# Optimization experiments

Measured on AMD Instinct MI355X. Metric: run time of the kernel, lower is better.

## Reference

```python
import jax, jax.numpy as jnp
import numpy as np

B, C, N = 4, 192, 4096
K = 16                      # avg degree
E = B * N * K               # 262144 edges
C_OUT = 384


def setup_inputs() -> dict:
    key = jax.random.key(0)
    k1, k2, k3, k4 = jax.random.split(key, 4)
    x = jax.random.normal(k1, (B, C, N, 1), dtype=jnp.float32)
    edge_index = jax.random.randint(k2, (2, E), 0, B * N, dtype=jnp.int64)
    # BasicConv([2C, C_OUT]): 1x1 Conv2d + bias + ReLU (norm=None)
    W = jax.random.normal(k3, (C_OUT, 2 * C), dtype=jnp.float32) * (1.0 / np.sqrt(2 * C))
    b = jax.random.normal(k4, (C_OUT,), dtype=jnp.float32) * 0.01
    return {"x": x, "edge_index": edge_index, "W": W, "b": b}


def reference(x, edge_index, W, b):
    Bs, Cs, Ns, _ = x.shape
    BN = Bs * Ns
    # (B,C,N,1) -> flattened node table (B*N, C); node id = b*N + n
    x_flat = jnp.transpose(x[..., 0], (0, 2, 1)).reshape(BN, Cs)
    x_i = x_flat[edge_index[0]]          # (E, C) gather at dst
    x_j = x_flat[edge_index[1]]          # (E, C) gather at src
    diff = x_j - x_i
    # scatter-max over dst nodes; torch_scatter fills empty segments with 0
    agg = jax.ops.segment_max(diff, edge_index[0], num_segments=BN)
    agg = jnp.where(jnp.isfinite(agg), agg, 0.0)
    x_j_out = jnp.transpose(agg.reshape(Bs, Ns, Cs), (0, 2, 1))[..., None]  # (B,C,N,1)
    # interleave channels: cat along new axis 2 then reshape -> (B, 2C, N, 1)
    cat = jnp.stack([x, x_j_out], axis=2).reshape(Bs, 2 * Cs, Ns, 1)
    # 1x1 conv == GEMM over channels, + bias + ReLU
    out = jnp.einsum('oc,bcnw->bonw', W, cat) + b[None, :, None, None]
    return jax.nn.relu(out)
```

## Files before the change

### kernel.cpp

```cpp
#include <hip/hip_runtime.h>
#include <hip/hip_bf16.h>
#include <math.h>

#define Bz    4
#define Cch   192
#define Nn    4096
#define BN    16384
#define Ecnt  262144
#define COUT  384
#define CAP   64

typedef __attribute__((ext_vector_type(8))) short short8;
typedef __attribute__((ext_vector_type(4))) float floatx4;

__device__ __forceinline__ void gload_lds16(const void* g, void* l) {
    __builtin_amdgcn_global_load_lds(
        (const __attribute__((address_space(1))) unsigned int*)g,
        (__attribute__((address_space(3))) unsigned int*)l, 16, 0, 0);
}

__device__ __forceinline__ float b2f(unsigned short u) {
    union { unsigned int i; float f; } z; z.i = ((unsigned int)u) << 16; return z.f;
}
__device__ __forceinline__ unsigned short f2b(float f) {
    __hip_bfloat16 h = __float2bfloat16(f);
    return *(unsigned short*)&h;
}

__global__ __launch_bounds__(256) void prep_kernel(
    const float* __restrict__ x, const unsigned int* __restrict__ ew,
    const float* __restrict__ W, __hip_bfloat16* __restrict__ xb,
    __hip_bfloat16* __restrict__ Wx, __hip_bfloat16* __restrict__ Wa,
    int* __restrict__ deg, int* __restrict__ flag) {
    int bid = blockIdx.x;
    if (bid < 3072) {
        __shared__ float tile[32][33];
        int b = bid / 768;
        int r = bid - b * 768;
        int c0 = (r >> 7) * 32;
        int n0 = (r & 127) * 32;
        int tx = threadIdx.x & 31, ty = threadIdx.x >> 5;
        for (int i = ty; i < 32; i += 8)
            tile[i][tx] = x[((size_t)(b * Cch + c0 + i)) * Nn + n0 + tx];
        __syncthreads();
        for (int i = ty; i < 32; i += 8)
            xb[((size_t)(b * Nn + n0 + i)) * Cch + c0 + tx] =
                __float2bfloat16(tile[tx][i]);
    } else if (bid < 3360) {
        int i = (bid - 3072) * 256 + threadIdx.x;
        int o = i / Cch, c = i - o * Cch;
        Wx[i] = __float2bfloat16(W[o * 2 * Cch + 2 * c]);
        Wa[i] = __float2bfloat16(W[o * 2 * Cch + 2 * c + 1]);
    } else if (bid < 3424) {
        deg[(bid - 3360) * 256 + threadIdx.x] = 0;
    } else {
        __shared__ int s;
        if (threadIdx.x == 0) s = 1;
        __syncthreads();
        if (ew[2 * threadIdx.x + 1] != 0u) atomicAnd(&s, 0);
        __syncthreads();
        if (threadIdx.x == 0) *flag = s;
    }
}

__global__ __launch_bounds__(256) void fill_kernel(
    const int* __restrict__ ew, const int* __restrict__ flag,
    int* __restrict__ deg, int* __restrict__ slots) {
    int t = blockIdx.x * 256 + threadIdx.x;
    int d0, d1, s0, s1;
    if (*flag) {
        int4 dv = *(const int4*)&ew[4 * t];
        int4 sv = *(const int4*)&ew[2 * Ecnt + 4 * t];
        d0 = dv.x; d1 = dv.z; s0 = sv.x; s1 = sv.z;
    } else {
        int2 dv = *(const int2*)&ew[2 * t];
        int2 sv = *(const int2*)&ew[Ecnt + 2 * t];
        d0 = dv.x; d1 = dv.y; s0 = sv.x; s1 = sv.y;
    }
    int p0 = atomicAdd(&deg[d0], 1); if (p0 < CAP) slots[(d0 << 6) + p0] = s0;
    int p1 = atomicAdd(&deg[d1], 1); if (p1 < CAP) slots[(d1 << 6) + p1] = s1;
}

__global__ __launch_bounds__(256) void agg_kernel(
    const int* __restrict__ deg, const int* __restrict__ slots,
    const __hip_bfloat16* __restrict__ xb, __hip_bfloat16* __restrict__ aggb) {
    int lane = threadIdx.x & 63, wave = threadIdx.x >> 6;
    int node = (blockIdx.x << 2) + wave;
    int d = deg[node]; if (d > CAP) d = CAP;
    int nbrval = 0;
    if (lane < d) nbrval = slots[(node << 6) + lane];
    const unsigned short* xbu = (const unsigned short*)xb;
    int act = lane < 48;
    int cb = lane * 4;
    float m0 = -INFINITY, m1 = -INFINITY, m2 = -INFINITY, m3 = -INFINITY;
    int k = 0;
    for (; k + 4 <= d; k += 4) {
        int s0 = __shfl(nbrval, k);
        int s1 = __shfl(nbrval, k + 1);
        int s2 = __shfl(nbrval, k + 2);
        int s3 = __shfl(nbrval, k + 3);
        if (act) {
            ushort4 v0 = *(const ushort4*)&xbu[s0 * Cch + cb];
            ushort4 v1 = *(const ushort4*)&xbu[s1 * Cch + cb];
            ushort4 v2 = *(const ushort4*)&xbu[s2 * Cch + cb];
            ushort4 v3 = *(const ushort4*)&xbu[s3 * Cch + cb];
            m0 = fmaxf(fmaxf(m0, b2f(v0.x)), fmaxf(fmaxf(b2f(v1.x), b2f(v2.x)), b2f(v3.x)));
            m1 = fmaxf(fmaxf(m1, b2f(v0.y)), fmaxf(fmaxf(b2f(v1.y), b2f(v2.y)), b2f(v3.y)));
            m2 = fmaxf(fmaxf(m2, b2f(v0.z)), fmaxf(fmaxf(b2f(v1.z), b2f(v2.z)), b2f(v3.z)));
            m3 = fmaxf(fmaxf(m3, b2f(v0.w)), fmaxf(fmaxf(b2f(v1.w), b2f(v2.w)), b2f(v3.w)));
        }
    }
    for (; k < d; k++) {
        int s = __shfl(nbrval, k);
        if (act) {
            ushort4 v = *(const ushort4*)&xbu[s * Cch + cb];
            m0 = fmaxf(m0, b2f(v.x)); m1 = fmaxf(m1, b2f(v.y));
            m2 = fmaxf(m2, b2f(v.z)); m3 = fmaxf(m3, b2f(v.w));
        }
    }
    if (act) {
        ushort4 xv = *(const ushort4*)&xbu[node * Cch + cb];
        ushort4 o4;
        o4.x = (d > 0) ? f2b(m0 - b2f(xv.x)) : 0;
        o4.y = (d > 0) ? f2b(m1 - b2f(xv.y)) : 0;
        o4.z = (d > 0) ? f2b(m2 - b2f(xv.z)) : 0;
        o4.w = (d > 0) ? f2b(m3 - b2f(xv.w)) : 0;
        *(ushort4*)&((unsigned short*)aggb)[node * Cch + cb] = o4;
    }
}

__global__ __launch_bounds__(256) void gemm_kernel(
    const __hip_bfloat16* __restrict__ Xb, const __hip_bfloat16* __restrict__ Ab,
    const __hip_bfloat16* __restrict__ Wx, const __hip_bfloat16* __restrict__ Wa,
    const float* __restrict__ bias, float* __restrict__ out) {
    __shared__ short As[64 * 32];
    __shared__ short Bs[64 * 32];
    int t = threadIdx.x;
    int node0 = blockIdx.x * 64;
    int o0    = blockIdx.y * 64;
    int lane = t & 63, wave = t >> 6;
    int quad = lane >> 4, lrow = lane & 15;
    int wm = wave & 1, wn = wave >> 1;

    floatx4 acc[2][2] = {};
    int srow = t >> 2;
    int koff = (t & 3) * 8;

    const __hip_bfloat16* Asrc[2] = {Xb, Ab};
    const __hip_bfloat16* Bsrc[2] = {Wx, Wa};

    for (int seg = 0; seg < 2; seg++) {
        const __hip_bfloat16* a_g = Asrc[seg] + (size_t)(node0 + srow) * Cch + koff;
        const __hip_bfloat16* b_g = Bsrc[seg] + (size_t)(o0 + srow) * Cch + koff;
        for (int kt = 0; kt < Cch; kt += 32) {
            __syncthreads();
            gload_lds16(a_g + kt, &As[t * 8]);
            gload_lds16(b_g + kt, &Bs[t * 8]);
            __syncthreads();
            short8 af0 = *(const short8*)&As[(wm * 32 + lrow) * 32 + quad * 8];
            short8 af1 = *(const short8*)&As[(wm * 32 + 16 + lrow) * 32 + quad * 8];
            short8 bf0 = *(const short8*)&Bs[(wn * 32 + lrow) * 32 + quad * 8];
            short8 bf1 = *(const short8*)&Bs[(wn * 32 + 16 + lrow) * 32 + quad * 8];
            acc[0][0] = __builtin_amdgcn_mfma_f32_16x16x32_bf16(bf0, af0, acc[0][0], 0, 0, 0);
            acc[1][0] = __builtin_amdgcn_mfma_f32_16x16x32_bf16(bf0, af1, acc[1][0], 0, 0, 0);
            acc[0][1] = __builtin_amdgcn_mfma_f32_16x16x32_bf16(bf1, af0, acc[0][1], 0, 0, 0);
            acc[1][1] = __builtin_amdgcn_mfma_f32_16x16x32_bf16(bf1, af1, acc[1][1], 0, 0, 0);
        }
    }

#pragma unroll
    for (int im = 0; im < 2; im++) {
        int node = node0 + wm * 32 + im * 16 + lrow;
        int b = node >> 12, n = node & 4095;
#pragma unroll
        for (int in = 0; in < 2; in++) {
            int ob = o0 + wn * 32 + in * 16 + quad * 4;
#pragma unroll
            for (int r = 0; r < 4; r++) {
                int o = ob + r;
                float v = acc[im][in][r] + bias[o];
                out[((size_t)(b * COUT + o)) * Nn + n] = fmaxf(v, 0.0f);
            }
        }
    }
}

extern "C" void kernel_launch(void* const* d_in, const int* in_sizes, int n_in,
                              void* d_out, int out_size, void* d_ws, size_t ws_size,
                              hipStream_t stream) {
    const float* x    = (const float*)d_in[0];
    const int*   ew   = (const int*)d_in[1];
    const float* W    = (const float*)d_in[2];
    const float* bias = (const float*)d_in[3];
    float* out        = (float*)d_out;

    char* ws = (char*)d_ws;
    __hip_bfloat16* xb   = (__hip_bfloat16*)ws;
    __hip_bfloat16* aggb = (__hip_bfloat16*)(ws + 6291456);
    __hip_bfloat16* Wx   = (__hip_bfloat16*)(ws + 12582912);
    __hip_bfloat16* Wa   = (__hip_bfloat16*)(ws + 12730368);
    int* deg   = (int*)(ws + 12877824);
    int* slots = (int*)(ws + 12943360);
    int* flag  = (int*)(ws + 17137664);

    prep_kernel<<<3425, 256, 0, stream>>>(x, (const unsigned int*)ew, W, xb, Wx, Wa, deg, flag);
    fill_kernel<<<Ecnt / 512, 256, 0, stream>>>(ew, flag, deg, slots);
    agg_kernel<<<BN / 4, 256, 0, stream>>>(deg, slots, xb, aggb);
    gemm_kernel<<<dim3(BN / 64, COUT / 64), 256, 0, stream>>>(xb, aggb, Wx, Wa, bias, out);
}
```

Before: 115.8 us.

## Fuse aggregation into GEMM via LDS and merge prep with edge fill

Each block now computes the max-aggregated neighbour features for its 64 nodes directly into a padded LDS tile and loops over all six output tiles, so the aggb buffer is never written to or read back from global memory. Edge slot filling moves into the prep kernel, with the format check done per block, and deg is zeroed by a memset, reducing four launches to two plus a memset. The GEMM grid shrinks from 1536 to 256 blocks with about 55KB of LDS each, which lowers parallelism and occupancy during the gather phase. The fill blocks now run in the same kernel as the x transpose that writes xb, but only the aggregation reads xb, so there is no race.

```diff
diff --git a/kernel.cpp b/kernel.cpp
--- a/kernel.cpp
+++ b/kernel.cpp
@@ -9,6 +9,7 @@
 #define Ecnt  262144
 #define COUT  384
 #define CAP   64
+#define PADW  392
 
 typedef __attribute__((ext_vector_type(8))) short short8;
 typedef __attribute__((ext_vector_type(4))) float floatx4;
@@ -27,11 +28,11 @@
     return *(unsigned short*)&h;
 }
 
-__global__ __launch_bounds__(256) void prep_kernel(
-    const float* __restrict__ x, const unsigned int* __restrict__ ew,
+__global__ __launch_bounds__(256) void prep_fill_kernel(
+    const float* __restrict__ x, const int* __restrict__ ew,
     const float* __restrict__ W, __hip_bfloat16* __restrict__ xb,
     __hip_bfloat16* __restrict__ Wx, __hip_bfloat16* __restrict__ Wa,
-    int* __restrict__ deg, int* __restrict__ flag) {
+    int* __restrict__ deg, int* __restrict__ slots) {
     int bid = blockIdx.x;
     if (bid < 3072) {
         __shared__ float tile[32][33];
@@ -51,111 +52,106 @@
         int o = i / Cch, c = i - o * Cch;
         Wx[i] = __float2bfloat16(W[o * 2 * Cch + 2 * c]);
         Wa[i] = __float2bfloat16(W[o * 2 * Cch + 2 * c + 1]);
-    } else if (bid < 3424) {
-        deg[(bid - 3360) * 256 + threadIdx.x] = 0;
     } else {
         __shared__ int s;
         if (threadIdx.x == 0) s = 1;
         __syncthreads();
-        if (ew[2 * threadIdx.x + 1] != 0u) atomicAnd(&s, 0);
+        if (((const unsigned int*)ew)[2 * threadIdx.x + 1] != 0u) atomicAnd(&s, 0);
         __syncthreads();
-        if (threadIdx.x == 0) *flag = s;
+        int is64 = s;
+        int t = (bid - 3360) * 256 + threadIdx.x;
+        int d0, d1, s0, s1;
+        if (is64) {
+            int4 dv = *(const int4*)&ew[4 * t];
+            int4 sv = *(const int4*)&ew[2 * Ecnt + 4 * t];
+            d0 = dv.x; d1 = dv.z; s0 = sv.x; s1 = sv.z;
+        } else {
+            int2 dv = *(const int2*)&ew[2 * t];
+            int2 sv = *(const int2*)&ew[Ecnt + 2 * t];
+            d0 = dv.x; d1 = dv.y; s0 = sv.x; s1 = sv.y;
+        }
+        int p0 = atomicAdd(&deg[d0], 1); if (p0 < CAP) slots[(d0 << 6) + p0] = s0;
+        int p1 = atomicAdd(&deg[d1], 1); if (p1 < CAP) slots[(d1 << 6) + p1] = s1;
     }
 }
 
-__global__ __launch_bounds__(256) void fill_kernel(
-    const int* __restrict__ ew, const int* __restrict__ flag,
-    int* __restrict__ deg, int* __restrict__ slots) {
-    int t = blockIdx.x * 256 + threadIdx.x;
-    int d0, d1, s0, s1;
-    if (*flag) {
-        int4 dv = *(const int4*)&ew[4 * t];
-        int4 sv = *(const int4*)&ew[2 * Ecnt + 4 * t];
-        d0 = dv.x; d1 = dv.z; s0 = sv.x; s1 = sv.z;
-    } else {
-        int2 dv = *(const int2*)&ew[2 * t];
-        int2 sv = *(const int2*)&ew[Ecnt + 2 * t];
-        d0 = dv.x; d1 = dv.y; s0 = sv.x; s1 = sv.y;
-    }
-    int p0 = atomicAdd(&deg[d0], 1); if (p0 < CAP) slots[(d0 << 6) + p0] = s0;
-    int p1 = atomicAdd(&deg[d1], 1); if (p1 < CAP) slots[(d1 << 6) + p1] = s1;
-}
-
-__global__ __launch_bounds__(256) void agg_kernel(
+__global__ __launch_bounds__(256) void agg_gemm_kernel(
     const int* __restrict__ deg, const int* __restrict__ slots,
-    const __hip_bfloat16* __restrict__ xb, __hip_bfloat16* __restrict__ aggb) {
-    int lane = threadIdx.x & 63, wave = threadIdx.x >> 6;
-    int node = (blockIdx.x << 2) + wave;
-    int d = deg[node]; if (d > CAP) d = CAP;
-    int nbrval = 0;
-    if (lane < d) nbrval = slots[(node << 6) + lane];
-    const unsigned short* xbu = (const unsigned short*)xb;
-    int act = lane < 48;
-    int cb = lane * 4;
-    float m0 = -INFINITY, m1 = -INFINITY, m2 = -INFINITY, m3 = -INFINITY;
-    int k = 0;
-    for (; k + 4 <= d; k += 4) {
-        int s0 = __shfl(nbrval, k);
-        int s1 = __shfl(nbrval, k + 1);
-        int s2 = __shfl(nbrval, k + 2);
-        int s3 = __shfl(nbrval, k + 3);
-        if (act) {
-            ushort4 v0 = *(const ushort4*)&xbu[s0 * Cch + cb];
-            ushort4 v1 = *(const ushort4*)&xbu[s1 * Cch + cb];
-            ushort4 v2 = *(const ushort4*)&xbu[s2 * Cch + cb];
-            ushort4 v3 = *(const ushort4*)&xbu[s3 * Cch + cb];
-            m0 = fmaxf(fmaxf(m0, b2f(v0.x)), fmaxf(fmaxf(b2f(v1.x), b2f(v2.x)), b2f(v3.x)));
-            m1 = fmaxf(fmaxf(m1, b2f(v0.y)), fmaxf(fmaxf(b2f(v1.y), b2f(v2.y)), b2f(v3.y)));
-            m2 = fmaxf(fmaxf(m2, b2f(v0.z)), fmaxf(fmaxf(b2f(v1.z), b2f(v2.z)), b2f(v3.z)));
-            m3 = fmaxf(fmaxf(m3, b2f(v0.w)), fmaxf(fmaxf(b2f(v1.w), b2f(v2.w)), b2f(v3.w)));
-        }
-    }
-    for (; k < d; k++) {
-        int s = __shfl(nbrval, k);
-        if (act) {
-            ushort4 v = *(const ushort4*)&xbu[s * Cch + cb];
-            m0 = fmaxf(m0, b2f(v.x)); m1 = fmaxf(m1, b2f(v.y));
-            m2 = fmaxf(m2, b2f(v.z)); m3 = fmaxf(m3, b2f(v.w));
-        }
-    }
-    if (act) {
-        ushort4 xv = *(const ushort4*)&xbu[node * Cch + cb];
-        ushort4 o4;
-        o4.x = (d > 0) ? f2b(m0 - b2f(xv.x)) : 0;
-        o4.y = (d > 0) ? f2b(m1 - b2f(xv.y)) : 0;
-        o4.z = (d > 0) ? f2b(m2 - b2f(xv.z)) : 0;
-        o4.w = (d > 0) ? f2b(m3 - b2f(xv.w)) : 0;
-        *(ushort4*)&((unsigned short*)aggb)[node * Cch + cb] = o4;
-    }
-}
-
-__global__ __launch_bounds__(256) void gemm_kernel(
-    const __hip_bfloat16* __restrict__ Xb, const __hip_bfloat16* __restrict__ Ab,
+    const __hip_bfloat16* __restrict__ xb,
     const __hip_bfloat16* __restrict__ Wx, const __hip_bfloat16* __restrict__ Wa,
     const float* __restrict__ bias, float* __restrict__ out) {
+    __shared__ unsigned short aggT[64 * PADW];
     __shared__ short As[64 * 32];
     __shared__ short Bs[64 * 32];
     int t = threadIdx.x;
+    int lane = t & 63, wave = t >> 6;
     int node0 = blockIdx.x * 64;
-    int o0    = blockIdx.y * 64;
-    int lane = t & 63, wave = t >> 6;
+
+    {
+        const unsigned short* xbu = (const unsigned short*)xb;
+        int act = lane < 48;
+        int cb = lane * 4;
+        for (int it = 0; it < 16; it++) {
+            int nl = wave * 16 + it;
+            int node = node0 + nl;
+            int d = deg[node]; if (d > CAP) d = CAP;
+            int nbrval = 0;
+            if (lane < d) nbrval = slots[(node << 6) + lane];
+            float m0 = -INFINITY, m1 = -INFINITY, m2 = -INFINITY, m3 = -INFINITY;
+            int k = 0;
+            for (; k + 4 <= d; k += 4) {
+                int s0 = __shfl(nbrval, k);
+                int s1 = __shfl(nbrval, k + 1);
+                int s2 = __shfl(nbrval, k + 2);
+                int s3 = __shfl(nbrval, k + 3);
+                if (act) {
+                    ushort4 v0 = *(const ushort4*)&xbu[s0 * Cch + cb];
+                    ushort4 v1 = *(const ushort4*)&xbu[s1 * Cch + cb];
+                    ushort4 v2 = *(const ushort4*)&xbu[s2 * Cch + cb];
+                    ushort4 v3 = *(const ushort4*)&xbu[s3 * Cch + cb];
+                    m0 = fmaxf(fmaxf(m0, b2f(v0.x)), fmaxf(fmaxf(b2f(v1.x), b2f(v2.x)), b2f(v3.x)));
+                    m1 = fmaxf(fmaxf(m1, b2f(v0.y)), fmaxf(fmaxf(b2f(v1.y), b2f(v2.y)), b2f(v3.y)));
+                    m2 = fmaxf(fmaxf(m2, b2f(v0.z)), fmaxf(fmaxf(b2f(v1.z), b2f(v2.z)), b2f(v3.z)));
+                    m3 = fmaxf(fmaxf(m3, b2f(v0.w)), fmaxf(fmaxf(b2f(v1.w), b2f(v2.w)), b2f(v3.w)));
+                }
+            }
+            for (; k < d; k++) {
+                int s = __shfl(nbrval, k);
+                if (act) {
+                    ushort4 v = *(const ushort4*)&xbu[s * Cch + cb];
+                    m0 = fmaxf(m0, b2f(v.x)); m1 = fmaxf(m1, b2f(v.y));
+                    m2 = fmaxf(m2, b2f(v.z)); m3 = fmaxf(m3, b2f(v.w));
+                }
+            }
+            if (act) {
+                ushort4 xv = *(const ushort4*)&xbu[node * Cch + cb];
+                ushort4 o4;
+                o4.x = (d > 0) ? f2b(m0 - b2f(xv.x)) : 0;
+                o4.y = (d > 0) ? f2b(m1 - b2f(xv.y)) : 0;
+                o4.z = (d > 0) ? f2b(m2 - b2f(xv.z)) : 0;
+                o4.w = (d > 0) ? f2b(m3 - b2f(xv.w)) : 0;
+                *(ushort4*)&aggT[nl * PADW + cb] = o4;
+            }
+        }
+    }
+    __syncthreads();
+
     int quad = lane >> 4, lrow = lane & 15;
     int wm = wave & 1, wn = wave >> 1;
-
-    floatx4 acc[2][2] = {};
     int srow = t >> 2;
     int koff = (t & 3) * 8;
-
-    const __hip_bfloat16* Asrc[2] = {Xb, Ab};
-    const __hip_bfloat16* Bsrc[2] = {Wx, Wa};
-
-    for (int seg = 0; seg < 2; seg++) {
-        const __hip_bfloat16* a_g = Asrc[seg] + (size_t)(node0 + srow) * Cch + koff;
-        const __hip_bfloat16* b_g = Bsrc[seg] + (size_t)(o0 + srow) * Cch + koff;
+    const __hip_bfloat16* a_g = xb + (size_t)(node0 + srow) * Cch + koff;
+
+    for (int ot = 0; ot < 6; ot++) {
+        int o0 = ot * 64;
+        floatx4 acc[2][2] = {};
+        const __hip_bfloat16* bx_g = Wx + (size_t)(o0 + srow) * Cch + koff;
+        const __hip_bfloat16* ba_g = Wa + (size_t)(o0 + srow) * Cch + koff;
+
         for (int kt = 0; kt < Cch; kt += 32) {
             __syncthreads();
-            gload_lds16(a_g + kt, &As[t * 8]);
-            gload_lds16(b_g + kt, &Bs[t * 8]);
+            gload_lds16(a_g + kt,  &As[t * 8]);
+            gload_lds16(bx_g + kt, &Bs[t * 8]);
             __syncthreads();
             short8 af0 = *(const short8*)&As[(wm * 32 + lrow) * 32 + quad * 8];
             short8 af1 = *(const short8*)&As[(wm * 32 + 16 + lrow) * 32 + quad * 8];
@@ -166,20 +162,33 @@
             acc[0][1] = __builtin_amdgcn_mfma_f32_16x16x32_bf16(bf1, af0, acc[0][1], 0, 0, 0);
             acc[1][1] = __builtin_amdgcn_mfma_f32_16x16x32_bf16(bf1, af1, acc[1][1], 0, 0, 0);
         }
-    }
+        for (int kt = 0; kt < Cch; kt += 32) {
+            __syncthreads();
+            gload_lds16(ba_g + kt, &Bs[t * 8]);
+            __syncthreads();
+            short8 af0 = *(const short8*)&aggT[(wm * 32 + lrow) * PADW + kt + quad * 8];
+            short8 af1 = *(const short8*)&aggT[(wm * 32 + 16 + lrow) * PADW + kt + quad * 8];
+            short8 bf0 = *(const short8*)&Bs[(wn * 32 + lrow) * 32 + quad * 8];
+            short8 bf1 = *(const short8*)&Bs[(wn * 32 + 16 + lrow) * 32 + quad * 8];
+            acc[0][0] = __builtin_amdgcn_mfma_f32_16x16x32_bf16(bf0, af0, acc[0][0], 0, 0, 0);
+            acc[1][0] = __builtin_amdgcn_mfma_f32_16x16x32_bf16(bf0, af1, acc[1][0], 0, 0, 0);
+            acc[0][1] = __builtin_amdgcn_mfma_f32_16x16x32_bf16(bf1, af0, acc[0][1], 0, 0, 0);
+            acc[1][1] = __builtin_amdgcn_mfma_f32_16x16x32_bf16(bf1, af1, acc[1][1], 0, 0, 0);
+        }
 
 #pragma unroll
-    for (int im = 0; im < 2; im++) {
-        int node = node0 + wm * 32 + im * 16 + lrow;
-        int b = node >> 12, n = node & 4095;
+        for (int im = 0; im < 2; im++) {
+            int node = node0 + wm * 32 + im * 16 + lrow;
+            int b = node >> 12, n = node & 4095;
 #pragma unroll
-        for (int in = 0; in < 2; in++) {
-            int ob = o0 + wn * 32 + in * 16 + quad * 4;
+            for (int in = 0; in < 2; in++) {
+                int ob = o0 + wn * 32 + in * 16 + quad * 4;
 #pragma unroll
-            for (int r = 0; r < 4; r++) {
-                int o = ob + r;
-                float v = acc[im][in][r] + bias[o];
-                out[((size_t)(b * COUT + o)) * Nn + n] = fmaxf(v, 0.0f);
+                for (int r = 0; r < 4; r++) {
+                    int o = ob + r;
+                    float v = acc[im][in][r] + bias[o];
+                    out[((size_t)(b * COUT + o)) * Nn + n] = fmaxf(v, 0.0f);
+                }
             }
         }
     }
@@ -196,15 +205,12 @@
 
     char* ws = (char*)d_ws;
     __hip_bfloat16* xb   = (__hip_bfloat16*)ws;
-    __hip_bfloat16* aggb = (__hip_bfloat16*)(ws + 6291456);
     __hip_bfloat16* Wx   = (__hip_bfloat16*)(ws + 12582912);
     __hip_bfloat16* Wa   = (__hip_bfloat16*)(ws + 12730368);
     int* deg   = (int*)(ws + 12877824);
     int* slots = (int*)(ws + 12943360);
-    int* flag  = (int*)(ws + 17137664);
-
-    prep_kernel<<<3425, 256, 0, stream>>>(x, (const unsigned int*)ew, W, xb, Wx, Wa, deg, flag);
-    fill_kernel<<<Ecnt / 512, 256, 0, stream>>>(ew, flag, deg, slots);
-    agg_kernel<<<BN / 4, 256, 0, stream>>>(deg, slots, xb, aggb);
-    gemm_kernel<<<dim3(BN / 64, COUT / 64), 256, 0, stream>>>(xb, aggb, Wx, Wa, bias, out);
-}
+
+    hipMemsetAsync(deg, 0, BN * sizeof(int), stream);
+    prep_fill_kernel<<<3872, 256, 0, stream>>>(x, ew, W, xb, Wx, Wa, deg, slots);
+    agg_gemm_kernel<<<BN / 64, 256, 0, stream>>>(deg, slots, xb, Wx, Wa, bias, out);
+}
```

After: 160.0 us. 38.2% more time.

## Fuse prep, fill, aggregate and GEMM into one persistent kernel with grid barriers

Applied to the files above, without the earlier changes.

Replaces the four separate launches with a single persistent kernel of 1024 blocks. Each block loops over the work of each former kernel, and atomic-counter grid barriers separate the phases. The degree counters and barrier counters are zeroed with one memset, and the fill phase runs alongside the transpose and weight conversion, so the separate prep stage and flag kernel are gone. This removes launch overhead and inter-kernel gaps. In exchange it relies on all 1024 blocks being co-resident, at 4 per CU under the launch bounds, or the barriers deadlock. Spin-waiting and the lower occupancy cap may also slow the GEMM and gather phases.

```diff
diff --git a/kernel.cpp b/kernel.cpp
--- a/kernel.cpp
+++ b/kernel.cpp
@@ -9,6 +9,7 @@
 #define Ecnt  262144
 #define COUT  384
 #define CAP   64
+#define GRID  1024
 
 typedef __attribute__((ext_vector_type(8))) short short8;
 typedef __attribute__((ext_vector_type(4))) float floatx4;
@@ -27,159 +28,168 @@
     return *(unsigned short*)&h;
 }
 
-__global__ __launch_bounds__(256) void prep_kernel(
-    const float* __restrict__ x, const unsigned int* __restrict__ ew,
-    const float* __restrict__ W, __hip_bfloat16* __restrict__ xb,
+__device__ __forceinline__ void grid_barrier(int* __restrict__ bar, int idx) {
+    __syncthreads();
+    if (threadIdx.x == 0) {
+        __threadfence();
+        int* c = bar + idx;
+        __hip_atomic_fetch_add(c, 1, __ATOMIC_ACQ_REL, __HIP_MEMORY_SCOPE_AGENT);
+        while (__hip_atomic_load(c, __ATOMIC_ACQUIRE, __HIP_MEMORY_SCOPE_AGENT) < GRID) {}
+        __threadfence();
+    }
+    __syncthreads();
+}
+
+__global__ __launch_bounds__(256, 4) void mono_kernel(
+    const float* __restrict__ x, const int* __restrict__ ew,
+    const float* __restrict__ W, const float* __restrict__ bias,
+    __hip_bfloat16* __restrict__ xb, __hip_bfloat16* __restrict__ aggb,
     __hip_bfloat16* __restrict__ Wx, __hip_bfloat16* __restrict__ Wa,
-    int* __restrict__ deg, int* __restrict__ flag) {
-    int bid = blockIdx.x;
-    if (bid < 3072) {
-        __shared__ float tile[32][33];
-        int b = bid / 768;
-        int r = bid - b * 768;
-        int c0 = (r >> 7) * 32;
-        int n0 = (r & 127) * 32;
-        int tx = threadIdx.x & 31, ty = threadIdx.x >> 5;
-        for (int i = ty; i < 32; i += 8)
-            tile[i][tx] = x[((size_t)(b * Cch + c0 + i)) * Nn + n0 + tx];
-        __syncthreads();
-        for (int i = ty; i < 32; i += 8)
-            xb[((size_t)(b * Nn + n0 + i)) * Cch + c0 + tx] =
-                __float2bfloat16(tile[tx][i]);
-    } else if (bid < 3360) {
-        int i = (bid - 3072) * 256 + threadIdx.x;
-        int o = i / Cch, c = i - o * Cch;
-        Wx[i] = __float2bfloat16(W[o * 2 * Cch + 2 * c]);
-        Wa[i] = __float2bfloat16(W[o * 2 * Cch + 2 * c + 1]);
-    } else if (bid < 3424) {
-        deg[(bid - 3360) * 256 + threadIdx.x] = 0;
-    } else {
-        __shared__ int s;
-        if (threadIdx.x == 0) s = 1;
-        __syncthreads();
-        if (ew[2 * threadIdx.x + 1] != 0u) atomicAnd(&s, 0);
-        __syncthreads();
-        if (threadIdx.x == 0) *flag = s;
-    }
-}
-
-__global__ __launch_bounds__(256) void fill_kernel(
-    const int* __restrict__ ew, const int* __restrict__ flag,
-    int* __restrict__ deg, int* __restrict__ slots) {
-    int t = blockIdx.x * 256 + threadIdx.x;
-    int d0, d1, s0, s1;
-    if (*flag) {
-        int4 dv = *(const int4*)&ew[4 * t];
-        int4 sv = *(const int4*)&ew[2 * Ecnt + 4 * t];
-        d0 = dv.x; d1 = dv.z; s0 = sv.x; s1 = sv.z;
-    } else {
-        int2 dv = *(const int2*)&ew[2 * t];
-        int2 sv = *(const int2*)&ew[Ecnt + 2 * t];
-        d0 = dv.x; d1 = dv.y; s0 = sv.x; s1 = sv.y;
-    }
-    int p0 = atomicAdd(&deg[d0], 1); if (p0 < CAP) slots[(d0 << 6) + p0] = s0;
-    int p1 = atomicAdd(&deg[d1], 1); if (p1 < CAP) slots[(d1 << 6) + p1] = s1;
-}
-
-__global__ __launch_bounds__(256) void agg_kernel(
-    const int* __restrict__ deg, const int* __restrict__ slots,
-    const __hip_bfloat16* __restrict__ xb, __hip_bfloat16* __restrict__ aggb) {
-    int lane = threadIdx.x & 63, wave = threadIdx.x >> 6;
-    int node = (blockIdx.x << 2) + wave;
-    int d = deg[node]; if (d > CAP) d = CAP;
-    int nbrval = 0;
-    if (lane < d) nbrval = slots[(node << 6) + lane];
-    const unsigned short* xbu = (const unsigned short*)xb;
-    int act = lane < 48;
-    int cb = lane * 4;
-    float m0 = -INFINITY, m1 = -INFINITY, m2 = -INFINITY, m3 = -INFINITY;
-    int k = 0;
-    for (; k + 4 <= d; k += 4) {
-        int s0 = __shfl(nbrval, k);
-        int s1 = __shfl(nbrval, k + 1);
-        int s2 = __shfl(nbrval, k + 2);
-        int s3 = __shfl(nbrval, k + 3);
-        if (act) {
-            ushort4 v0 = *(const ushort4*)&xbu[s0 * Cch + cb];
-            ushort4 v1 = *(const ushort4*)&xbu[s1 * Cch + cb];
-            ushort4 v2 = *(const ushort4*)&xbu[s2 * Cch + cb];
-            ushort4 v3 = *(const ushort4*)&xbu[s3 * Cch + cb];
-            m0 = fmaxf(fmaxf(m0, b2f(v0.x)), fmaxf(fmaxf(b2f(v1.x), b2f(v2.x)), b2f(v3.x)));
-            m1 = fmaxf(fmaxf(m1, b2f(v0.y)), fmaxf(fmaxf(b2f(v1.y), b2f(v2.y)), b2f(v3.y)));
-            m2 = fmaxf(fmaxf(m2, b2f(v0.z)), fmaxf(fmaxf(b2f(v1.z), b2f(v2.z)), b2f(v3.z)));
-            m3 = fmaxf(fmaxf(m3, b2f(v0.w)), fmaxf(fmaxf(b2f(v1.w), b2f(v2.w)), b2f(v3.w)));
-        }
-    }
-    for (; k < d; k++) {
-        int s = __shfl(nbrval, k);
-        if (act) {
-            ushort4 v = *(const ushort4*)&xbu[s * Cch + cb];
-            m0 = fmaxf(m0, b2f(v.x)); m1 = fmaxf(m1, b2f(v.y));
-            m2 = fmaxf(m2, b2f(v.z)); m3 = fmaxf(m3, b2f(v.w));
-        }
-    }
-    if (act) {
-        ushort4 xv = *(const ushort4*)&xbu[node * Cch + cb];
-        ushort4 o4;
-        o4.x = (d > 0) ? f2b(m0 - b2f(xv.x)) : 0;
-        o4.y = (d > 0) ? f2b(m1 - b2f(xv.y)) : 0;
-        o4.z = (d > 0) ? f2b(m2 - b2f(xv.z)) : 0;
-        o4.w = (d > 0) ? f2b(m3 - b2f(xv.w)) : 0;
-        *(ushort4*)&((unsigned short*)aggb)[node * Cch + cb] = o4;
-    }
-}
-
-__global__ __launch_bounds__(256) void gemm_kernel(
-    const __hip_bfloat16* __restrict__ Xb, const __hip_bfloat16* __restrict__ Ab,
-    const __hip_bfloat16* __restrict__ Wx, const __hip_bfloat16* __restrict__ Wa,
-    const float* __restrict__ bias, float* __restrict__ out) {
+    int* __restrict__ deg, int* __restrict__ slots, int* __restrict__ bar,
+    float* __restrict__ out) {
+    __shared__ float tileT[32][33];
     __shared__ short As[64 * 32];
     __shared__ short Bs[64 * 32];
+    __shared__ int s_is64;
     int t = threadIdx.x;
-    int node0 = blockIdx.x * 64;
-    int o0    = blockIdx.y * 64;
+    int bid = blockIdx.x;
     int lane = t & 63, wave = t >> 6;
-    int quad = lane >> 4, lrow = lane & 15;
-    int wm = wave & 1, wn = wave >> 1;
-
-    floatx4 acc[2][2] = {};
-    int srow = t >> 2;
-    int koff = (t & 3) * 8;
-
-    const __hip_bfloat16* Asrc[2] = {Xb, Ab};
-    const __hip_bfloat16* Bsrc[2] = {Wx, Wa};
-
-    for (int seg = 0; seg < 2; seg++) {
-        const __hip_bfloat16* a_g = Asrc[seg] + (size_t)(node0 + srow) * Cch + koff;
-        const __hip_bfloat16* b_g = Bsrc[seg] + (size_t)(o0 + srow) * Cch + koff;
-        for (int kt = 0; kt < Cch; kt += 32) {
+
+    if (t == 0) s_is64 = 1;
+    __syncthreads();
+    if (((const unsigned int*)ew)[2 * t + 1] != 0u) atomicAnd(&s_is64, 0);
+    __syncthreads();
+    int is64 = s_is64;
+
+    for (int u = bid; u < 3872; u += GRID) {
+        if (u < 3072) {
+            int b = u / 768;
+            int r = u - b * 768;
+            int c0 = (r >> 7) * 32;
+            int n0 = (r & 127) * 32;
+            int tx = t & 31, ty = t >> 5;
             __syncthreads();
-            gload_lds16(a_g + kt, &As[t * 8]);
-            gload_lds16(b_g + kt, &Bs[t * 8]);
+            for (int i = ty; i < 32; i += 8)
+                tileT[i][tx] = x[((size_t)(b * Cch + c0 + i)) * Nn + n0 + tx];
             __syncthreads();
-            short8 af0 = *(const short8*)&As[(wm * 32 + lrow) * 32 + quad * 8];
-            short8 af1 = *(const short8*)&As[(wm * 32 + 16 + lrow) * 32 + quad * 8];
-            short8 bf0 = *(const short8*)&Bs[(wn * 32 + lrow) * 32 + quad * 8];
-            short8 bf1 = *(const short8*)&Bs[(wn * 32 + 16 + lrow) * 32 + quad * 8];
-            acc[0][0] = __builtin_amdgcn_mfma_f32_16x16x32_bf16(bf0, af0, acc[0][0], 0, 0, 0);
-            acc[1][0] = __builtin_amdgcn_mfma_f32_16x16x32_bf16(bf0, af1, acc[1][0], 0, 0, 0);
-            acc[0][1] = __builtin_amdgcn_mfma_f32_16x16x32_bf16(bf1, af0, acc[0][1], 0, 0, 0);
-            acc[1][1] = __builtin_amdgcn_mfma_f32_16x16x32_bf16(bf1, af1, acc[1][1], 0, 0, 0);
+            for (int i = ty; i < 32; i += 8)
+                xb[((size_t)(b * Nn + n0 + i)) * Cch + c0 + tx] =
+                    __float2bfloat16(tileT[tx][i]);
+        } else if (u < 3360) {
+            int i = (u - 3072) * 256 + t;
+            int o = i / Cch, c = i - o * Cch;
+            Wx[i] = __float2bfloat16(W[o * 2 * Cch + 2 * c]);
+            Wa[i] = __float2bfloat16(W[o * 2 * Cch + 2 * c + 1]);
+        } else {
+            int te = (u - 3360) * 256 + t;
+            int d0, d1, s0, s1;
+            if (is64) {
+                int4 dv = *(const int4*)&ew[4 * te];
+                int4 sv = *(const int4*)&ew[2 * Ecnt + 4 * te];
+                d0 = dv.x; d1 = dv.z; s0 = sv.x; s1 = sv.z;
+            } else {
+                int2 dv = *(const int2*)&ew[2 * te];
+                int2 sv = *(const int2*)&ew[Ecnt + 2 * te];
+                d0 = dv.x; d1 = dv.y; s0 = sv.x; s1 = sv.y;
+            }
+            int p0 = atomicAdd(&deg[d0], 1); if (p0 < CAP) slots[(d0 << 6) + p0] = s0;
+            int p1 = atomicAdd(&deg[d1], 1); if (p1 < CAP) slots[(d1 << 6) + p1] = s1;
         }
     }
-
+    grid_barrier(bar, 0);
+
+    {
+        const unsigned short* xbu = (const unsigned short*)xb;
+        int act = lane < 48;
+        int cb = lane * 4;
+        for (int u = bid; u < 4096; u += GRID) {
+            int node = (u << 2) + wave;
+            int d = deg[node]; if (d > CAP) d = CAP;
+            int nbrval = 0;
+            if (lane < d) nbrval = slots[(node << 6) + lane];
+            float m0 = -INFINITY, m1 = -INFINITY, m2 = -INFINITY, m3 = -INFINITY;
+            int k = 0;
+            for (; k + 4 <= d; k += 4) {
+                int s0 = __shfl(nbrval, k);
+                int s1 = __shfl(nbrval, k + 1);
+                int s2 = __shfl(nbrval, k + 2);
+                int s3 = __shfl(nbrval, k + 3);
+                if (act) {
+                    ushort4 v0 = *(const ushort4*)&xbu[s0 * Cch + cb];
+                    ushort4 v1 = *(const ushort4*)&xbu[s1 * Cch + cb];
+                    ushort4 v2 = *(const ushort4*)&xbu[s2 * Cch + cb];
+                    ushort4 v3 = *(const ushort4*)&xbu[s3 * Cch + cb];
+                    m0 = fmaxf(fmaxf(m0, b2f(v0.x)), fmaxf(fmaxf(b2f(v1.x), b2f(v2.x)), b2f(v3.x)));
+                    m1 = fmaxf(fmaxf(m1, b2f(v0.y)), fmaxf(fmaxf(b2f(v1.y), b2f(v2.y)), b2f(v3.y)));
+                    m2 = fmaxf(fmaxf(m2, b2f(v0.z)), fmaxf(fmaxf(b2f(v1.z), b2f(v2.z)), b2f(v3.z)));
+                    m3 = fmaxf(fmaxf(m3, b2f(v0.w)), fmaxf(fmaxf(b2f(v1.w), b2f(v2.w)), b2f(v3.w)));
+                }
+            }
+            for (; k < d; k++) {
+                int s = __shfl(nbrval, k);
+                if (act) {
+                    ushort4 v = *(const ushort4*)&xbu[s * Cch + cb];
+                    m0 = fmaxf(m0, b2f(v.x)); m1 = fmaxf(m1, b2f(v.y));
+                    m2 = fmaxf(m2, b2f(v.z)); m3 = fmaxf(m3, b2f(v.w));
+                }
+            }
+            if (act) {
+                ushort4 xv = *(const ushort4*)&xbu[node * Cch + cb];
+                ushort4 o4;
+                o4.x = (d > 0) ? f2b(m0 - b2f(xv.x)) : 0;
+                o4.y = (d > 0) ? f2b(m1 - b2f(xv.y)) : 0;
+                o4.z = (d > 0) ? f2b(m2 - b2f(xv.z)) : 0;
+                o4.w = (d > 0) ? f2b(m3 - b2f(xv.w)) : 0;
+                *(ushort4*)&((unsigned short*)aggb)[node * Cch + cb] = o4;
+            }
+        }
+    }
+    grid_barrier(bar, 1);
+
+    {
+        int quad = lane >> 4, lrow = lane & 15;
+        int wm = wave & 1, wn = wave >> 1;
+        int srow = t >> 2;
+        int koff = (t & 3) * 8;
+        const __hip_bfloat16* Asrc[2] = {xb, aggb};
+        const __hip_bfloat16* Bsrc[2] = {Wx, Wa};
+
+        for (int u = bid; u < 1536; u += GRID) {
+            int node0 = (u & 255) * 64;
+            int o0    = (u >> 8) * 64;
+            floatx4 acc[2][2] = {};
+            for (int seg = 0; seg < 2; seg++) {
+                const __hip_bfloat16* a_g = Asrc[seg] + (size_t)(node0 + srow) * Cch + koff;
+                const __hip_bfloat16* b_g = Bsrc[seg] + (size_t)(o0 + srow) * Cch + koff;
+                for (int kt = 0; kt < Cch; kt += 32) {
+                    __syncthreads();
+                    gload_lds16(a_g + kt, &As[t * 8]);
+                    gload_lds16(b_g + kt, &Bs[t * 8]);
+                    __syncthreads();
+                    short8 af0 = *(const short8*)&As[(wm * 32 + lrow) * 32 + quad * 8];
+                    short8 af1 = *(const short8*)&As[(wm * 32 + 16 + lrow) * 32 + quad * 8];
+                    short8 bf0 = *(const short8*)&Bs[(wn * 32 + lrow) * 32 + quad * 8];
+                    short8 bf1 = *(const short8*)&Bs[(wn * 32 + 16 + lrow) * 32 + quad * 8];
+                    acc[0][0] = __builtin_amdgcn_mfma_f32_16x16x32_bf16(bf0, af0, acc[0][0], 0, 0, 0);
+                    acc[1][0] = __builtin_amdgcn_mfma_f32_16x16x32_bf16(bf0, af1, acc[1][0], 0, 0, 0);
+                    acc[0][1] = __builtin_amdgcn_mfma_f32_16x16x32_bf16(bf1, af0, acc[0][1], 0, 0, 0);
+                    acc[1][1] = __builtin_amdgcn_mfma_f32_16x16x32_bf16(bf1, af1, acc[1][1], 0, 0, 0);
+                }
+            }
 #pragma unroll
-    for (int im = 0; im < 2; im++) {
-        int node = node0 + wm * 32 + im * 16 + lrow;
-        int b = node >> 12, n = node & 4095;
+            for (int im = 0; im < 2; im++) {
+                int node = node0 + wm * 32 + im * 16 + lrow;
+                int b = node >> 12, n = node & 4095;
 #pragma unroll
-        for (int in = 0; in < 2; in++) {
-            int ob = o0 + wn * 32 + in * 16 + quad * 4;
+                for (int in = 0; in < 2; in++) {
+                    int ob = o0 + wn * 32 + in * 16 + quad * 4;
 #pragma unroll
-            for (int r = 0; r < 4; r++) {
-                int o = ob + r;
-                float v = acc[im][in][r] + bias[o];
-                out[((size_t)(b * COUT + o)) * Nn + n] = fmaxf(v, 0.0f);
+                    for (int r = 0; r < 4; r++) {
+                        int o = ob + r;
+                        float v = acc[im][in][r] + bias[o];
+                        out[((size_t)(b * COUT + o)) * Nn + n] = fmaxf(v, 0.0f);
+                    }
+                }
             }
         }
     }
@@ -200,11 +210,10 @@
     __hip_bfloat16* Wx   = (__hip_bfloat16*)(ws + 12582912);
     __hip_bfloat16* Wa   = (__hip_bfloat16*)(ws + 12730368);
     int* deg   = (int*)(ws + 12877824);
-    int* slots = (int*)(ws + 12943360);
-    int* flag  = (int*)(ws + 17137664);
-
-    prep_kernel<<<3425, 256, 0, stream>>>(x, (const unsigned int*)ew, W, xb, Wx, Wa, deg, flag);
-    fill_kernel<<<Ecnt / 512, 256, 0, stream>>>(ew, flag, deg, slots);
-    agg_kernel<<<BN / 4, 256, 0, stream>>>(deg, slots, xb, aggb);
-    gemm_kernel<<<dim3(BN / 64, COUT / 64), 256, 0, stream>>>(xb, aggb, Wx, Wa, bias, out);
-}
+    int* bar   = (int*)(ws + 12943360);
+    int* slots = (int*)(ws + 12943424);
+
+    hipMemsetAsync(deg, 0, 65536 + 64, stream);
+    mono_kernel<<<GRID, 256, 0, stream>>>(x, ew, W, bias, xb, aggb, Wx, Wa,
+                                          deg, slots, bar, out);
+}
```

Measured after the change: 434.8 us. +275.6%, slower.
